# Performance work log

Measured on AMD Instinct MI355X. Metric: run time of the kernel, lower is better.

The kernel has to match this reference:

```python
import jax, jax.numpy as jnp
import numpy as np

INPUT_DIM = 20000
UNITS = 4096
NNZ = 2_000_000
BATCH = 2048


def setup_inputs() -> dict:
    key = jax.random.key(0)
    k1, k2, k3, k4 = jax.random.split(key, 4)
    x = jax.random.normal(k1, (BATCH, INPUT_DIM), dtype=jnp.float32)
    kernel_vector = jax.random.normal(k2, (NNZ,), dtype=jnp.float32) * 0.05
    bias = jnp.zeros((UNITS,), dtype=jnp.float32)
    rows = jax.random.randint(k3, (NNZ,), 0, INPUT_DIM, dtype=jnp.int32)
    cols = jax.random.randint(k4, (NNZ,), 0, UNITS, dtype=jnp.int32)
    nonzero_ind = jnp.stack([rows, cols], axis=1)  # (NNZ, 2)
    return {"x": x, "kernel_vector": kernel_vector, "bias": bias, "nonzero_ind": nonzero_ind}


def reference(x, kernel_vector, bias, nonzero_ind):
    # scatter_nd: build dense (input_dim, units) kernel from COO representation.
    # Duplicate indices accumulate (tf.scatter_nd semantics) -> use .add.
    trans = jnp.zeros((INPUT_DIM, UNITS), dtype=kernel_vector.dtype)
    trans = trans.at[nonzero_ind[:, 0], nonzero_ind[:, 1]].add(kernel_vector)
    out = x @ trans + bias  # (batch, units)
    return jnp.tanh(out)
```

## Files before the change

### kernel.cpp

```cpp
#include <hip/hip_runtime.h>
#include <cstdint>
#include <cstddef>

#define M_DIM 2048
#define N_DIM 4096
#define K_DIM 20000
#define KP    20480
#define KZ    10240
#define NTILE 160
#define WBT_BYTES  167772160UL
#define XB_OFFSET  167772160UL
#define CP_OFFSET  251658240UL

typedef __attribute__((ext_vector_type(8))) short short8;
typedef __attribute__((ext_vector_type(2))) short short2v;
typedef __attribute__((ext_vector_type(4))) float float4v;
typedef __attribute__((ext_vector_type(8))) unsigned short ushort8;

__device__ __forceinline__ unsigned short f2bf_rne(float f) {
    union { float f; unsigned int u; } v; v.f = f;
    unsigned int u = v.u;
    u += 0x7FFFu + ((u >> 16) & 1u);
    return (unsigned short)(u >> 16);
}

__device__ __forceinline__ float bf2f(unsigned short h) {
    union { unsigned int u; float f; } v;
    v.u = ((unsigned int)h) << 16;
    return v.f;
}

__device__ __forceinline__ void gload_lds16(const void* g, void* l) {
    __builtin_amdgcn_global_load_lds(
        (const __attribute__((address_space(1))) void*)g,
        (__attribute__((address_space(3))) void*)l, 16, 0, 0);
}

__global__ void zero_wbt_kernel(float4* __restrict__ p) {
    size_t t = (size_t)blockIdx.x * 256 + threadIdx.x;
    float4 z; z.x = 0.f; z.y = 0.f; z.z = 0.f; z.w = 0.f;
    #pragma unroll
    for (int i = 0; i < 20; ++i)
        p[t + (size_t)i * (2048 * 256)] = z;
}

__global__ void scatter_bf16_kernel(const float* __restrict__ kv,
                                    const int* __restrict__ ind,
                                    unsigned int* __restrict__ W, int nnz) {
    int t = blockIdx.x * blockDim.x + threadIdx.x;
    if (t >= nnz) return;
    int r = ind[2 * t];
    int c = ind[2 * t + 1];
    float v = kv[t];
    size_t elem = (size_t)c * KP + r;
    unsigned int* word = &W[elem >> 1];
    const bool hi = (elem & 1) != 0;
    unsigned short hbits = f2bf_rne(v);
#if __has_builtin(__builtin_amdgcn_global_atomic_fadd_v2bf16)
    short2v val;
    val[0] = hi ? (short)0 : (short)hbits;
    val[1] = hi ? (short)hbits : (short)0;
    __builtin_amdgcn_global_atomic_fadd_v2bf16(
        (__attribute__((address_space(1))) short2v*)word, val);
#else
    unsigned int expected = 0u;
    unsigned int desired  = hi ? ((unsigned int)hbits << 16) : (unsigned int)hbits;
    for (;;) {
        unsigned int old = atomicCAS(word, expected, desired);
        if (old == expected) break;
        expected = old;
        unsigned short hcur = hi ? (unsigned short)(old >> 16)
                                 : (unsigned short)(old & 0xFFFFu);
        unsigned short nh = f2bf_rne(bf2f(hcur) + v);
        desired = hi ? ((old & 0x0000FFFFu) | ((unsigned int)nh << 16))
                     : ((old & 0xFFFF0000u) | (unsigned int)nh);
    }
#endif
}

__global__ void convert_kernel(const float* __restrict__ src,
                               unsigned short* __restrict__ dst) {
    size_t t = (size_t)blockIdx.x * 256 + threadIdx.x;
    int row = (int)(t / 2560);
    int c8  = (int)(t % 2560);
    ushort8 o;
    if (c8 < 2500) {
        const float4* sv = (const float4*)(src + (size_t)row * K_DIM + (size_t)c8 * 8);
        float4 a = sv[0];
        float4 b = sv[1];
        o[0] = f2bf_rne(a.x); o[1] = f2bf_rne(a.y);
        o[2] = f2bf_rne(a.z); o[3] = f2bf_rne(a.w);
        o[4] = f2bf_rne(b.x); o[5] = f2bf_rne(b.y);
        o[6] = f2bf_rne(b.z); o[7] = f2bf_rne(b.w);
    } else {
        o = (ushort8)0;
    }
    *(ushort8*)(dst + (size_t)row * KP + (size_t)c8 * 8) = o;
}

__global__ __launch_bounds__(512, 2) void gemm256_kernel(
    const unsigned short* __restrict__ A,
    const unsigned short* __restrict__ Bt,
    float* __restrict__ Cp) {

    __shared__ unsigned short L[65536];

    const int t    = threadIdx.x;
    const int w    = t >> 6;
    const int l    = t & 63;
    const int quad = l >> 4;
    const int r16  = l & 15;
    const int wm   = w >> 2;
    const int wn   = w & 3;

    const int m0 = blockIdx.y * 256;
    const int n0 = blockIdx.x * 256;
    const size_t k0 = (size_t)blockIdx.z * KZ;

    const int lr8 = l >> 3;
    const int sl  = (l & 7) ^ lr8;
    const int w1024 = w << 10;

    const unsigned short* pA0 = A  + (size_t)(m0 +   0 + w * 8 + lr8) * KP + k0 + sl * 8;
    const unsigned short* pA1 = A  + (size_t)(m0 +  64 + w * 8 + lr8) * KP + k0 + sl * 8;
    const unsigned short* pA2 = A  + (size_t)(m0 + 128 + w * 8 + lr8) * KP + k0 + sl * 8;
    const unsigned short* pA3 = A  + (size_t)(m0 + 192 + w * 8 + lr8) * KP + k0 + sl * 8;
    const unsigned short* pB0 = Bt + (size_t)(n0 +   0 + w * 8 + lr8) * KP + k0 + sl * 8;
    const unsigned short* pB1 = Bt + (size_t)(n0 +  64 + w * 8 + lr8) * KP + k0 + sl * 8;
    const unsigned short* pB2 = Bt + (size_t)(n0 + 128 + w * 8 + lr8) * KP + k0 + sl * 8;
    const unsigned short* pB3 = Bt + (size_t)(n0 + 192 + w * 8 + lr8) * KP + k0 + sl * 8;

    char* Lb = (char*)L;

#define STG_A(OB, Q, P) do { \
    gload_lds16(P, Lb + (OB) + (Q) * 8192 + w1024); P += 64; } while (0)
#define STG_B(OB, Q, P) do { \
    gload_lds16(P, Lb + (OB) + 32768 + (Q) * 8192 + w1024); P += 64; } while (0)

    const int h   = r16 & 7;
    const int so0 = ((quad ^ h) << 4);
    const int so1 = (((4 | quad) ^ h) << 4);
    const int aoff = wm * 16384 + r16 * 128;
    const int boff = 32768 + wn * 8192 + r16 * 128;

    float4v acc[8][4];
#pragma unroll
    for (int i = 0; i < 8; ++i)
#pragma unroll
        for (int j = 0; j < 4; ++j)
            acc[i][j] = (float4v){0.f, 0.f, 0.f, 0.f};

    short8 bfr[4], af[4];

#define VM2 asm volatile("s_waitcnt vmcnt(2)" ::: "memory")
#define VMNONE ((void)0)

#define PHASE(BUF, MH, SO, LOADB, STG, VM) do { \
    const char* base_ = Lb + (BUF); \
    if (LOADB) { \
        _Pragma("unroll") \
        for (int j = 0; j < 4; ++j) \
            bfr[j] = *(const short8*)(base_ + boff + j * 2048 + (SO)); \
    } \
    _Pragma("unroll") \
    for (int i = 0; i < 4; ++i) \
        af[i] = *(const short8*)(base_ + aoff + (MH) * 8192 + i * 2048 + (SO)); \
    STG; \
    __builtin_amdgcn_s_barrier(); \
    asm volatile("s_waitcnt lgkmcnt(0)" ::: "memory"); \
    __builtin_amdgcn_s_setprio(1); \
    _Pragma("unroll") \
    for (int i = 0; i < 4; ++i) \
        _Pragma("unroll") \
        for (int j = 0; j < 4; ++j) \
            acc[(MH) * 4 + i][j] = __builtin_amdgcn_mfma_f32_16x16x32_bf16( \
                af[i], bfr[j], acc[(MH) * 4 + i][j], 0, 0, 0); \
    __builtin_amdgcn_s_setprio(0); \
    VM; \
    __builtin_amdgcn_s_barrier(); \
} while (0)

#define TILE(BUF, OB) do { \
    PHASE(BUF, 0, so0, true,  { STG_A(OB, 0, pA0); STG_A(OB, 1, pA1); }, VMNONE); \
    PHASE(BUF, 1, so0, false, { STG_A(OB, 2, pA2); STG_A(OB, 3, pA3); }, VMNONE); \
    PHASE(BUF, 0, so1, true,  { STG_B(OB, 2, pB2); STG_B(OB, 3, pB3); }, VMNONE); \
    PHASE(BUF, 1, so1, false, { STG_B(BUF, 0, pB0); STG_B(BUF, 1, pB1); }, VM2); \
} while (0)

    STG_A(0, 0, pA0); STG_A(0, 1, pA1); STG_A(0, 2, pA2); STG_A(0, 3, pA3);
    STG_B(0, 0, pB0); STG_B(0, 1, pB1); STG_B(0, 2, pB2); STG_B(0, 3, pB3);
    STG_B(65536, 0, pB0); STG_B(65536, 1, pB1);
    asm volatile("s_waitcnt vmcnt(2)" ::: "memory");
    __builtin_amdgcn_s_barrier();

#pragma unroll 1
    for (int it = 0; it < NTILE / 2; ++it) {
        TILE(0, 65536);
        TILE(65536, 0);
    }
    asm volatile("s_waitcnt vmcnt(0)" ::: "memory");

    float* Cz = Cp + (size_t)blockIdx.z * ((size_t)M_DIM * N_DIM);
#pragma unroll
    for (int i = 0; i < 8; ++i) {
        const int row = m0 + wm * 128 + i * 16 + quad * 4;
#pragma unroll
        for (int j = 0; j < 4; ++j) {
            const int col = n0 + wn * 64 + j * 16 + r16;
#pragma unroll
            for (int r = 0; r < 4; ++r)
                Cz[(size_t)(row + r) * N_DIM + col] = acc[i][j][r];
        }
    }
#undef TILE
#undef PHASE
#undef STG_A
#undef STG_B
#undef VM2
#undef VMNONE
}

__global__ void combine_kernel(const float* __restrict__ Cp,
                               const float* __restrict__ bias,
                               float* __restrict__ out) {
    size_t t = (size_t)blockIdx.x * 256 + threadIdx.x;
    const size_t stride = (size_t)M_DIM * N_DIM / 4;
    float4 a = ((const float4*)Cp)[t];
    float4 b = ((const float4*)Cp)[t + stride];
    float4 bv = ((const float4*)bias)[t & (N_DIM / 4 - 1)];
    float4 o;
    o.x = tanhf(a.x + b.x + bv.x);
    o.y = tanhf(a.y + b.y + bv.y);
    o.z = tanhf(a.z + b.z + bv.z);
    o.w = tanhf(a.w + b.w + bv.w);
    ((float4*)out)[t] = o;
}

extern "C" void kernel_launch(void* const* d_in, const int* in_sizes, int n_in,
                              void* d_out, int out_size, void* d_ws, size_t ws_size,
                              hipStream_t stream) {
    const float* x    = (const float*)d_in[0];
    const float* kv   = (const float*)d_in[1];
    const float* bias = (const float*)d_in[2];
    const int*   ind  = (const int*)d_in[3];
    const int nnz = in_sizes[1];

    unsigned short* Wbt = (unsigned short*)d_ws;
    unsigned short* xb  = (unsigned short*)((char*)d_ws + XB_OFFSET);
    float* Cp = (float*)((char*)d_ws + CP_OFFSET);

    zero_wbt_kernel<<<2048, 256, 0, stream>>>((float4*)Wbt);
    scatter_bf16_kernel<<<(nnz + 255) / 256, 256, 0, stream>>>(
        kv, ind, (unsigned int*)Wbt, nnz);
    convert_kernel<<<(M_DIM * (KP / 8)) / 256, 256, 0, stream>>>(x, xb);
    gemm256_kernel<<<dim3(N_DIM / 256, M_DIM / 256, 2), 512, 0, stream>>>(
        xb, Wbt, Cp);
    combine_kernel<<<(M_DIM * N_DIM) / (256 * 4), 256, 0, stream>>>(
        Cp, bias, (float*)d_out);
}
```

Measured before the change: 646.1 us.

## Replace split-K 256x256 GEMM with full-K 256x128 tiles and fused bias-tanh epilogue

Drops the two-way split-K over 256x256 tiles and runs full K on 256x128 output tiles. The grid stays at 256 blocks, the same count as before. Bias add and tanh are fused into the GEMM epilogue, which removes the fp32 partial-sum buffer writes and the separate combine kernel launch. In exchange each block gets less reuse per LDS load, because the narrower N tile raises the ratio of A loads to MFMA work. Each block's serial K loop also becomes twice as long, so any tail imbalance lasts longer.

```diff
diff --git a/kernel.cpp b/kernel.cpp
--- a/kernel.cpp
+++ b/kernel.cpp
@@ -6,11 +6,9 @@
 #define N_DIM 4096
 #define K_DIM 20000
 #define KP    20480
-#define KZ    10240
-#define NTILE 160
+#define NTILEF 320
 #define WBT_BYTES  167772160UL
 #define XB_OFFSET  167772160UL
-#define CP_OFFSET  251658240UL
 
 typedef __attribute__((ext_vector_type(8))) short short8;
 typedef __attribute__((ext_vector_type(2))) short short2v;
@@ -98,37 +96,35 @@
     *(ushort8*)(dst + (size_t)row * KP + (size_t)c8 * 8) = o;
 }
 
-__global__ __launch_bounds__(512, 2) void gemm256_kernel(
+__global__ __launch_bounds__(512, 2) void gemm_fullk_kernel(
     const unsigned short* __restrict__ A,
     const unsigned short* __restrict__ Bt,
-    float* __restrict__ Cp) {
-
-    __shared__ unsigned short L[65536];
+    const float* __restrict__ bias,
+    float* __restrict__ out) {
+
+    __shared__ unsigned short L[49152];
 
     const int t    = threadIdx.x;
     const int w    = t >> 6;
     const int l    = t & 63;
     const int quad = l >> 4;
     const int r16  = l & 15;
-    const int wm   = w >> 2;
-    const int wn   = w & 3;
+    const int wm   = w >> 1;
+    const int wn   = w & 1;
 
     const int m0 = blockIdx.y * 256;
-    const int n0 = blockIdx.x * 256;
-    const size_t k0 = (size_t)blockIdx.z * KZ;
+    const int n0 = blockIdx.x * 128;
 
     const int lr8 = l >> 3;
     const int sl  = (l & 7) ^ lr8;
     const int w1024 = w << 10;
 
-    const unsigned short* pA0 = A  + (size_t)(m0 +   0 + w * 8 + lr8) * KP + k0 + sl * 8;
-    const unsigned short* pA1 = A  + (size_t)(m0 +  64 + w * 8 + lr8) * KP + k0 + sl * 8;
-    const unsigned short* pA2 = A  + (size_t)(m0 + 128 + w * 8 + lr8) * KP + k0 + sl * 8;
-    const unsigned short* pA3 = A  + (size_t)(m0 + 192 + w * 8 + lr8) * KP + k0 + sl * 8;
-    const unsigned short* pB0 = Bt + (size_t)(n0 +   0 + w * 8 + lr8) * KP + k0 + sl * 8;
-    const unsigned short* pB1 = Bt + (size_t)(n0 +  64 + w * 8 + lr8) * KP + k0 + sl * 8;
-    const unsigned short* pB2 = Bt + (size_t)(n0 + 128 + w * 8 + lr8) * KP + k0 + sl * 8;
-    const unsigned short* pB3 = Bt + (size_t)(n0 + 192 + w * 8 + lr8) * KP + k0 + sl * 8;
+    const unsigned short* pA0 = A  + (size_t)(m0 +   0 + w * 8 + lr8) * KP + sl * 8;
+    const unsigned short* pA1 = A  + (size_t)(m0 +  64 + w * 8 + lr8) * KP + sl * 8;
+    const unsigned short* pA2 = A  + (size_t)(m0 + 128 + w * 8 + lr8) * KP + sl * 8;
+    const unsigned short* pA3 = A  + (size_t)(m0 + 192 + w * 8 + lr8) * KP + sl * 8;
+    const unsigned short* pB0 = Bt + (size_t)(n0 +   0 + w * 8 + lr8) * KP + sl * 8;
+    const unsigned short* pB1 = Bt + (size_t)(n0 +  64 + w * 8 + lr8) * KP + sl * 8;
 
     char* Lb = (char*)L;
 
@@ -140,100 +136,95 @@
     const int h   = r16 & 7;
     const int so0 = ((quad ^ h) << 4);
     const int so1 = (((4 | quad) ^ h) << 4);
-    const int aoff = wm * 16384 + r16 * 128;
+    const int aoff = wm * 8192 + r16 * 128;
     const int boff = 32768 + wn * 8192 + r16 * 128;
 
-    float4v acc[8][4];
-#pragma unroll
-    for (int i = 0; i < 8; ++i)
+    float4v acc[4][4];
+#pragma unroll
+    for (int i = 0; i < 4; ++i)
 #pragma unroll
         for (int j = 0; j < 4; ++j)
             acc[i][j] = (float4v){0.f, 0.f, 0.f, 0.f};
 
-    short8 bfr[4], af[4];
+    short8 bfr[4][2], af[4];
 
 #define VM2 asm volatile("s_waitcnt vmcnt(2)" ::: "memory")
-#define VMNONE ((void)0)
-
-#define PHASE(BUF, MH, SO, LOADB, STG, VM) do { \
-    const char* base_ = Lb + (BUF); \
-    if (LOADB) { \
-        _Pragma("unroll") \
-        for (int j = 0; j < 4; ++j) \
-            bfr[j] = *(const short8*)(base_ + boff + j * 2048 + (SO)); \
+
+#define TILE(BUF, OB) do { \
+    {  \
+      const char* base_ = Lb + (BUF); \
+      _Pragma("unroll") \
+      for (int j = 0; j < 4; ++j) { \
+          bfr[j][0] = *(const short8*)(base_ + boff + j * 2048 + so0); \
+          bfr[j][1] = *(const short8*)(base_ + boff + j * 2048 + so1); \
+      } \
+      _Pragma("unroll") \
+      for (int i = 0; i < 4; ++i) \
+          af[i] = *(const short8*)(base_ + aoff + i * 2048 + so0); \
+      STG_A(OB, 0, pA0); STG_A(OB, 1, pA1); \
+      STG_A(OB, 2, pA2); STG_A(OB, 3, pA3); \
+      __builtin_amdgcn_s_barrier(); \
+      asm volatile("s_waitcnt lgkmcnt(0)" ::: "memory"); \
+      __builtin_amdgcn_s_setprio(1); \
+      _Pragma("unroll") \
+      for (int i = 0; i < 4; ++i) \
+          _Pragma("unroll") \
+          for (int j = 0; j < 4; ++j) \
+              acc[i][j] = __builtin_amdgcn_mfma_f32_16x16x32_bf16( \
+                  af[i], bfr[j][0], acc[i][j], 0, 0, 0); \
+      __builtin_amdgcn_s_setprio(0); \
+      __builtin_amdgcn_s_barrier(); \
     } \
-    _Pragma("unroll") \
-    for (int i = 0; i < 4; ++i) \
-        af[i] = *(const short8*)(base_ + aoff + (MH) * 8192 + i * 2048 + (SO)); \
-    STG; \
-    __builtin_amdgcn_s_barrier(); \
-    asm volatile("s_waitcnt lgkmcnt(0)" ::: "memory"); \
-    __builtin_amdgcn_s_setprio(1); \
-    _Pragma("unroll") \
-    for (int i = 0; i < 4; ++i) \
-        _Pragma("unroll") \
-        for (int j = 0; j < 4; ++j) \
-            acc[(MH) * 4 + i][j] = __builtin_amdgcn_mfma_f32_16x16x32_bf16( \
-                af[i], bfr[j], acc[(MH) * 4 + i][j], 0, 0, 0); \
-    __builtin_amdgcn_s_setprio(0); \
-    VM; \
-    __builtin_amdgcn_s_barrier(); \
+    {  \
+      const char* base_ = Lb + (BUF); \
+      _Pragma("unroll") \
+      for (int i = 0; i < 4; ++i) \
+          af[i] = *(const short8*)(base_ + aoff + i * 2048 + so1); \
+      STG_B(BUF, 0, pB0); STG_B(BUF, 1, pB1); \
+      __builtin_amdgcn_s_barrier(); \
+      asm volatile("s_waitcnt lgkmcnt(0)" ::: "memory"); \
+      __builtin_amdgcn_s_setprio(1); \
+      _Pragma("unroll") \
+      for (int i = 0; i < 4; ++i) \
+          _Pragma("unroll") \
+          for (int j = 0; j < 4; ++j) \
+              acc[i][j] = __builtin_amdgcn_mfma_f32_16x16x32_bf16( \
+                  af[i], bfr[j][1], acc[i][j], 0, 0, 0); \
+      __builtin_amdgcn_s_setprio(0); \
+      VM2; \
+      __builtin_amdgcn_s_barrier(); \
+    } \
 } while (0)
 
-#define TILE(BUF, OB) do { \
-    PHASE(BUF, 0, so0, true,  { STG_A(OB, 0, pA0); STG_A(OB, 1, pA1); }, VMNONE); \
-    PHASE(BUF, 1, so0, false, { STG_A(OB, 2, pA2); STG_A(OB, 3, pA3); }, VMNONE); \
-    PHASE(BUF, 0, so1, true,  { STG_B(OB, 2, pB2); STG_B(OB, 3, pB3); }, VMNONE); \
-    PHASE(BUF, 1, so1, false, { STG_B(BUF, 0, pB0); STG_B(BUF, 1, pB1); }, VM2); \
-} while (0)
-
     STG_A(0, 0, pA0); STG_A(0, 1, pA1); STG_A(0, 2, pA2); STG_A(0, 3, pA3);
-    STG_B(0, 0, pB0); STG_B(0, 1, pB1); STG_B(0, 2, pB2); STG_B(0, 3, pB3);
-    STG_B(65536, 0, pB0); STG_B(65536, 1, pB1);
+    STG_B(0, 0, pB0); STG_B(0, 1, pB1);
+    STG_B(49152, 0, pB0); STG_B(49152, 1, pB1);
     asm volatile("s_waitcnt vmcnt(2)" ::: "memory");
     __builtin_amdgcn_s_barrier();
 
 #pragma unroll 1
-    for (int it = 0; it < NTILE / 2; ++it) {
-        TILE(0, 65536);
-        TILE(65536, 0);
+    for (int it = 0; it < NTILEF / 2; ++it) {
+        TILE(0, 49152);
+        TILE(49152, 0);
     }
     asm volatile("s_waitcnt vmcnt(0)" ::: "memory");
 
-    float* Cz = Cp + (size_t)blockIdx.z * ((size_t)M_DIM * N_DIM);
-#pragma unroll
-    for (int i = 0; i < 8; ++i) {
-        const int row = m0 + wm * 128 + i * 16 + quad * 4;
-#pragma unroll
-        for (int j = 0; j < 4; ++j) {
-            const int col = n0 + wn * 64 + j * 16 + r16;
+#pragma unroll
+    for (int j = 0; j < 4; ++j) {
+        const int col = n0 + wn * 64 + j * 16 + r16;
+        const float bv = bias[col];
+#pragma unroll
+        for (int i = 0; i < 4; ++i) {
+            const int row = m0 + wm * 64 + i * 16 + quad * 4;
 #pragma unroll
             for (int r = 0; r < 4; ++r)
-                Cz[(size_t)(row + r) * N_DIM + col] = acc[i][j][r];
+                out[(size_t)(row + r) * N_DIM + col] = tanhf(acc[i][j][r] + bv);
         }
     }
 #undef TILE
-#undef PHASE
 #undef STG_A
 #undef STG_B
 #undef VM2
-#undef VMNONE
-}
-
-__global__ void combine_kernel(const float* __restrict__ Cp,
-                               const float* __restrict__ bias,
-                               float* __restrict__ out) {
-    size_t t = (size_t)blockIdx.x * 256 + threadIdx.x;
-    const size_t stride = (size_t)M_DIM * N_DIM / 4;
-    float4 a = ((const float4*)Cp)[t];
-    float4 b = ((const float4*)Cp)[t + stride];
-    float4 bv = ((const float4*)bias)[t & (N_DIM / 4 - 1)];
-    float4 o;
-    o.x = tanhf(a.x + b.x + bv.x);
-    o.y = tanhf(a.y + b.y + bv.y);
-    o.z = tanhf(a.z + b.z + bv.z);
-    o.w = tanhf(a.w + b.w + bv.w);
-    ((float4*)out)[t] = o;
 }
 
 extern "C" void kernel_launch(void* const* d_in, const int* in_sizes, int n_in,
@@ -247,14 +238,11 @@
 
     unsigned short* Wbt = (unsigned short*)d_ws;
     unsigned short* xb  = (unsigned short*)((char*)d_ws + XB_OFFSET);
-    float* Cp = (float*)((char*)d_ws + CP_OFFSET);
 
     zero_wbt_kernel<<<2048, 256, 0, stream>>>((float4*)Wbt);
     scatter_bf16_kernel<<<(nnz + 255) / 256, 256, 0, stream>>>(
         kv, ind, (unsigned int*)Wbt, nnz);
     convert_kernel<<<(M_DIM * (KP / 8)) / 256, 256, 0, stream>>>(x, xb);
-    gemm256_kernel<<<dim3(N_DIM / 256, M_DIM / 256, 2), 512, 0, stream>>>(
-        xb, Wbt, Cp);
-    combine_kernel<<<(M_DIM * N_DIM) / (256 * 4), 256, 0, stream>>>(
-        Cp, bias, (float*)d_out);
-}
+    gemm_fullk_kernel<<<dim3(N_DIM / 128, M_DIM / 256), 512, 0, stream>>>(
+        xb, Wbt, bias, (float*)d_out);
+}
```

Measured after the change: 676.0 us. +4.6%, slower.

## Fuse zero, scatter and x conversion into one cooperative prep kernel

Applied to the files above, without the earlier changes.

Replaces three separate launches (zeroing the bf16 weight buffer, atomic scatter of COO values, fp32-to-bf16 conversion of x) with one cooperative kernel of 1024 blocks. A grid-wide sync separates the zeroing from the scatter, and the x conversion runs after the scatter in the same threads. The aim is to remove launch gaps and tail effects between the small kernels. The cost is a grid barrier and lower parallelism, since each thread now loops over many elements with a fixed grid size.

```diff
diff --git a/kernel.cpp b/kernel.cpp
--- a/kernel.cpp
+++ b/kernel.cpp
@@ -1,6 +1,9 @@
 #include <hip/hip_runtime.h>
+#include <hip/hip_cooperative_groups.h>
 #include <cstdint>
 #include <cstddef>
+
+namespace cg = cooperative_groups;
 
 #define M_DIM 2048
 #define N_DIM 4096
@@ -11,6 +14,7 @@
 #define WBT_BYTES  167772160UL
 #define XB_OFFSET  167772160UL
 #define CP_OFFSET  251658240UL
+#define PREP_T 262144
 
 typedef __attribute__((ext_vector_type(8))) short short8;
 typedef __attribute__((ext_vector_type(2))) short short2v;
@@ -36,66 +40,77 @@
         (__attribute__((address_space(3))) void*)l, 16, 0, 0);
 }
 
-__global__ void zero_wbt_kernel(float4* __restrict__ p) {
-    size_t t = (size_t)blockIdx.x * 256 + threadIdx.x;
+__global__ void prep_kernel(const float* __restrict__ x,
+                            unsigned short* __restrict__ xb,
+                            float4* __restrict__ wz,
+                            const float* __restrict__ kv,
+                            const int* __restrict__ ind,
+                            unsigned int* __restrict__ W,
+                            int nnz) {
+    const size_t t = (size_t)blockIdx.x * 256 + threadIdx.x;
+
     float4 z; z.x = 0.f; z.y = 0.f; z.z = 0.f; z.w = 0.f;
     #pragma unroll
-    for (int i = 0; i < 20; ++i)
-        p[t + (size_t)i * (2048 * 256)] = z;
-}
-
-__global__ void scatter_bf16_kernel(const float* __restrict__ kv,
-                                    const int* __restrict__ ind,
-                                    unsigned int* __restrict__ W, int nnz) {
-    int t = blockIdx.x * blockDim.x + threadIdx.x;
-    if (t >= nnz) return;
-    int r = ind[2 * t];
-    int c = ind[2 * t + 1];
-    float v = kv[t];
-    size_t elem = (size_t)c * KP + r;
-    unsigned int* word = &W[elem >> 1];
-    const bool hi = (elem & 1) != 0;
-    unsigned short hbits = f2bf_rne(v);
+    for (int i = 0; i < 40; ++i)
+        wz[t + (size_t)i * PREP_T] = z;
+
+    __threadfence();
+    cg::this_grid().sync();
+
+    #pragma unroll
+    for (int i = 0; i < 8; ++i) {
+        size_t idx = t + (size_t)i * PREP_T;
+        if (idx < (size_t)nnz) {
+            int r = ind[2 * idx];
+            int c = ind[2 * idx + 1];
+            float v = kv[idx];
+            size_t elem = (size_t)c * KP + r;
+            unsigned int* word = &W[elem >> 1];
+            const bool hi = (elem & 1) != 0;
+            unsigned short hbits = f2bf_rne(v);
 #if __has_builtin(__builtin_amdgcn_global_atomic_fadd_v2bf16)
-    short2v val;
-    val[0] = hi ? (short)0 : (short)hbits;
-    val[1] = hi ? (short)hbits : (short)0;
-    __builtin_amdgcn_global_atomic_fadd_v2bf16(
-        (__attribute__((address_space(1))) short2v*)word, val);
+            short2v val;
+            val[0] = hi ? (short)0 : (short)hbits;
+            val[1] = hi ? (short)hbits : (short)0;
+            __builtin_amdgcn_global_atomic_fadd_v2bf16(
+                (__attribute__((address_space(1))) short2v*)word, val);
 #else
-    unsigned int expected = 0u;
-    unsigned int desired  = hi ? ((unsigned int)hbits << 16) : (unsigned int)hbits;
-    for (;;) {
-        unsigned int old = atomicCAS(word, expected, desired);
-        if (old == expected) break;
-        expected = old;
-        unsigned short hcur = hi ? (unsigned short)(old >> 16)
-                                 : (unsigned short)(old & 0xFFFFu);
-        unsigned short nh = f2bf_rne(bf2f(hcur) + v);
-        desired = hi ? ((old & 0x0000FFFFu) | ((unsigned int)nh << 16))
-                     : ((old & 0xFFFF0000u) | (unsigned int)nh);
-    }
+            unsigned int expected = 0u;
+            unsigned int desired  = hi ? ((unsigned int)hbits << 16)
+                                       : (unsigned int)hbits;
+            for (;;) {
+                unsigned int old = atomicCAS(word, expected, desired);
+                if (old == expected) break;
+                expected = old;
+                unsigned short hcur = hi ? (unsigned short)(old >> 16)
+                                         : (unsigned short)(old & 0xFFFFu);
+                unsigned short nh = f2bf_rne(bf2f(hcur) + v);
+                desired = hi ? ((old & 0x0000FFFFu) | ((unsigned int)nh << 16))
+                             : ((old & 0xFFFF0000u) | (unsigned int)nh);
+            }
 #endif
-}
-
-__global__ void convert_kernel(const float* __restrict__ src,
-                               unsigned short* __restrict__ dst) {
-    size_t t = (size_t)blockIdx.x * 256 + threadIdx.x;
-    int row = (int)(t / 2560);
-    int c8  = (int)(t % 2560);
-    ushort8 o;
-    if (c8 < 2500) {
-        const float4* sv = (const float4*)(src + (size_t)row * K_DIM + (size_t)c8 * 8);
-        float4 a = sv[0];
-        float4 b = sv[1];
-        o[0] = f2bf_rne(a.x); o[1] = f2bf_rne(a.y);
-        o[2] = f2bf_rne(a.z); o[3] = f2bf_rne(a.w);
-        o[4] = f2bf_rne(b.x); o[5] = f2bf_rne(b.y);
-        o[6] = f2bf_rne(b.z); o[7] = f2bf_rne(b.w);
-    } else {
-        o = (ushort8)0;
-    }
-    *(ushort8*)(dst + (size_t)row * KP + (size_t)c8 * 8) = o;
+        }
+    }
+
+    #pragma unroll
+    for (int i = 0; i < 20; ++i) {
+        size_t s = t + (size_t)i * PREP_T;
+        int row = (int)(s / 2560);
+        int c8  = (int)(s % 2560);
+        ushort8 o;
+        if (c8 < 2500) {
+            const float4* sv = (const float4*)(x + (size_t)row * K_DIM + (size_t)c8 * 8);
+            float4 a = sv[0];
+            float4 b = sv[1];
+            o[0] = f2bf_rne(a.x); o[1] = f2bf_rne(a.y);
+            o[2] = f2bf_rne(a.z); o[3] = f2bf_rne(a.w);
+            o[4] = f2bf_rne(b.x); o[5] = f2bf_rne(b.y);
+            o[6] = f2bf_rne(b.z); o[7] = f2bf_rne(b.w);
+        } else {
+            o = (ushort8)0;
+        }
+        *(ushort8*)(xb + (size_t)row * KP + (size_t)c8 * 8) = o;
+    }
 }
 
 __global__ __launch_bounds__(512, 2) void gemm256_kernel(
@@ -243,16 +258,22 @@
     const float* kv   = (const float*)d_in[1];
     const float* bias = (const float*)d_in[2];
     const int*   ind  = (const int*)d_in[3];
-    const int nnz = in_sizes[1];
+    int nnz = in_sizes[1];
 
     unsigned short* Wbt = (unsigned short*)d_ws;
     unsigned short* xb  = (unsigned short*)((char*)d_ws + XB_OFFSET);
     float* Cp = (float*)((char*)d_ws + CP_OFFSET);
 
-    zero_wbt_kernel<<<2048, 256, 0, stream>>>((float4*)Wbt);
-    scatter_bf16_kernel<<<(nnz + 255) / 256, 256, 0, stream>>>(
-        kv, ind, (unsigned int*)Wbt, nnz);
-    convert_kernel<<<(M_DIM * (KP / 8)) / 256, 256, 0, stream>>>(x, xb);
+    {
+        const float* xa = x; unsigned short* xba = xb;
+        float4* wza = (float4*)Wbt;
+        const float* kva = kv; const int* inda = ind;
+        unsigned int* Wa = (unsigned int*)Wbt;
+        void* args[] = { (void*)&xa, (void*)&xba, (void*)&wza,
+                         (void*)&kva, (void*)&inda, (void*)&Wa, (void*)&nnz };
+        hipLaunchCooperativeKernel((void*)prep_kernel, dim3(1024), dim3(256),
+                                   args, 0, stream);
+    }
     gemm256_kernel<<<dim3(N_DIM / 256, M_DIM / 256, 2), 512, 0, stream>>>(
         xb, Wbt, Cp);
     combine_kernel<<<(M_DIM * N_DIM) / (256 * 4), 256, 0, stream>>>(
```

New measurement: 877.9 us. +35.9%, slower.
